# Kernel optimization log

Measured on AMD Instinct MI355X. Metric: run time of the kernel, lower is better.

The kernel has to match this reference:

```python
import jax, jax.numpy as jnp
import numpy as np

D_MODEL = 1024
H = 16
D_K = D_MODEL // H


def setup_inputs() -> dict:
    key = jax.random.key(0)
    ks = jax.random.split(key, 11)
    B, S = 4, 2048
    scale = 1.0 / np.sqrt(D_MODEL)
    inp = {
        "q": jax.random.normal(ks[0], (B, S, D_MODEL), jnp.float32),
        "k": jax.random.normal(ks[1], (B, S, D_MODEL), jnp.float32),
        "v": jax.random.normal(ks[2], (B, S, D_MODEL), jnp.float32),
        "wq": jax.random.normal(ks[3], (D_MODEL, D_MODEL), jnp.float32) * scale,
        "bq": jax.random.normal(ks[4], (D_MODEL,), jnp.float32) * 0.02,
        "wk": jax.random.normal(ks[5], (D_MODEL, D_MODEL), jnp.float32) * scale,
        "bk": jax.random.normal(ks[6], (D_MODEL,), jnp.float32) * 0.02,
        "wv": jax.random.normal(ks[7], (D_MODEL, D_MODEL), jnp.float32) * scale,
        "bv": jax.random.normal(ks[8], (D_MODEL,), jnp.float32) * 0.02,
        "wo": jax.random.normal(ks[9], (D_MODEL, D_MODEL), jnp.float32) * scale,
        "bo": jax.random.normal(ks[10], (D_MODEL,), jnp.float32) * 0.02,
    }
    return inp


def _split_heads(x):
    b, s, d = x.shape
    return x.reshape(b, s, H, D_K).transpose(0, 2, 1, 3)  # b h s k


def reference(q, k, v, wq, bq, wk, bk, wv, bv, wo, bo):
    # linear projections (torch Linear: x @ W^T + b; here weights stored as [in,out])
    qh = _split_heads(q @ wq + bq)
    kh = _split_heads(k @ wk + bk)
    vh = _split_heads(v @ wv + bv)
    scores = jnp.einsum('bhsk,bhtk->bhst', qh, kh) / np.sqrt(D_K)
    attn = jax.nn.softmax(scores, axis=-1)
    wv_ = jnp.einsum('bhst,bhtk->bhsk', attn, vh)
    b, h, s, dk = wv_.shape
    cv = wv_.transpose(0, 2, 1, 3).reshape(b, s, h * dk)
    return cv @ wo + bo
```

## Files before the change

### kernel.cpp

```cpp
#include <hip/hip_runtime.h>


#define DM 1024
#define SQL 2048

typedef __attribute__((ext_vector_type(4))) float floatx4;
typedef __attribute__((ext_vector_type(8))) __bf16 bf16x8;
typedef __attribute__((ext_vector_type(4))) __bf16 bf16x4;
typedef __attribute__((ext_vector_type(4))) unsigned int uintx4;

#define SW(row, chunk) (((row) << 6) + ((((chunk) ^ ((row) & 7))) << 3))

#define GLD(gaddr, laddr)                                                              \
  __builtin_amdgcn_global_load_lds(                                                    \
      (const __attribute__((address_space(1))) unsigned int*)(gaddr),                  \
      (__attribute__((address_space(3))) unsigned int*)(laddr), 16, 0, 0)

__device__ __forceinline__ unsigned short f2bf(float f) {
  unsigned int u = __float_as_uint(f);
  u += 0x7fffu + ((u >> 16) & 1u);
  return (unsigned short)(u >> 16);
}

__device__ __forceinline__ unsigned int pack_bf(float lo, float hi) {
  unsigned int a = __float_as_uint(lo) + 0x8000u;
  unsigned int b = __float_as_uint(hi) + 0x8000u;
  return __builtin_amdgcn_perm(b, a, 0x07060302u);
}

__device__ __forceinline__ bf16x8 pack8(floatx4 a, floatx4 b) {
  bf16x8 r;
  r[0] = (__bf16)a[0]; r[1] = (__bf16)a[1]; r[2] = (__bf16)a[2]; r[3] = (__bf16)a[3];
  r[4] = (__bf16)b[0]; r[5] = (__bf16)b[1]; r[6] = (__bf16)b[2]; r[7] = (__bf16)b[3];
  return r;
}

__global__ __launch_bounds__(256) void transpose4_kernel(
    const float* __restrict__ w0, const float* __restrict__ w1,
    const float* __restrict__ w2, const float* __restrict__ w3,
    unsigned short* __restrict__ t0, unsigned short* __restrict__ t1,
    unsigned short* __restrict__ t2, unsigned short* __restrict__ t3) {
  __shared__ unsigned short t[64][65];
  int z = blockIdx.z;
  const float* W = (z == 0) ? w0 : (z == 1) ? w1 : (z == 2) ? w2 : w3;
  unsigned short* Wt = (z == 0) ? t0 : (z == 1) ? t1 : (z == 2) ? t2 : t3;
  int tid = threadIdx.x;
  int n0 = blockIdx.x * 64, k0 = blockIdx.y * 64;
  for (int u = 0; u < 16; u++) {
    int idx = u * 256 + tid;
    int k = idx >> 6, n = idx & 63;
    t[k][n] = f2bf(W[(size_t)(k0 + k) * DM + n0 + n]);
  }
  __syncthreads();
  for (int u = 0; u < 16; u++) {
    int idx = u * 256 + tid;
    int n = idx >> 6, k = idx & 63;
    Wt[(size_t)(n0 + n) * DM + k0 + k] = t[k][n];
  }
}

__global__ __launch_bounds__(256) void convert3_kernel(
    const float* __restrict__ s0, const float* __restrict__ s1,
    const float* __restrict__ s2, unsigned short* __restrict__ d0,
    unsigned short* __restrict__ d1, unsigned short* __restrict__ d2) {
  int z = blockIdx.y;
  const float* S = (z == 0) ? s0 : (z == 1) ? s1 : s2;
  unsigned short* D = (z == 0) ? d0 : (z == 1) ? d1 : d2;
  int t = blockIdx.x * 256 + threadIdx.x;
  for (int u = 0; u < 8; u++) {
    int i = (u << 18) + t;
    float4 vv = ((const float4*)S)[i];
    uint2 p;
    p.x = pack_bf(vv.x, vv.y);
    p.y = pack_bf(vv.z, vv.w);
    ((uint2*)D)[i] = p;
  }
}

__device__ __forceinline__ void gemm_core_256x128(
    const unsigned short* __restrict__ A, const unsigned short* __restrict__ Bt,
    int m0, int n0, unsigned short* lds_a, unsigned short* lds_b,
    floatx4 acc[4][4]) {
  int tid = threadIdx.x;
  int wave = tid >> 6, lane = tid & 63;
  int quad = lane >> 4, c16 = lane & 15;
  int wm = wave >> 1, wn = wave & 1;
  int r8 = lane >> 3, l8 = lane & 7;
  int xch = (l8 ^ r8) << 3;

  int r7 = c16 & 7;
  int aoff0 = ((wm * 64 + c16) << 6) + ((quad ^ r7) << 3);
  int aoff1 = ((wm * 64 + c16) << 6) + (((4 + quad) ^ r7) << 3);
  int boff0 = ((wn * 64 + c16) << 6) + ((quad ^ r7) << 3);
  int boff1 = ((wn * 64 + c16) << 6) + (((4 + quad) ^ r7) << 3);

  int aq = wave * 4;
  int bq = wave * 2;

#define STG_A(bufp, kt, u) \
  GLD(&A[(size_t)(m0 + (aq + (u)) * 8 + r8) * DM + (kt) + xch], (bufp) + (aq + (u)) * 512)
#define STG_B(bufp, kt, u) \
  GLD(&Bt[(size_t)(n0 + (bq + (u)) * 8 + r8) * DM + (kt) + xch], (bufp) + (bq + (u)) * 512)

  const floatx4 fz = {0.f, 0.f, 0.f, 0.f};
#pragma unroll
  for (int i = 0; i < 4; i++)
#pragma unroll
    for (int j = 0; j < 4; j++) acc[i][j] = fz;

#pragma unroll
  for (int u = 0; u < 4; u++) STG_A(lds_a, 0, u);
  STG_B(lds_b, 0, 0);
  STG_B(lds_b, 0, 1);
#pragma unroll
  for (int u = 0; u < 4; u++) STG_A(lds_a + 16384, 64, u);
  STG_B(lds_b + 8192, 64, 0);
  STG_B(lds_b + 8192, 64, 1);

  int cur = 0;
#pragma unroll 1
  for (int t = 0; t < 16; ++t) {
    if (t < 15) asm volatile("s_waitcnt vmcnt(6)\n\ts_barrier" ::: "memory");
    else        asm volatile("s_waitcnt vmcnt(0)\n\ts_barrier" ::: "memory");

    const unsigned short* la = lds_a + cur * 16384;
    const unsigned short* lb = lds_b + cur * 8192;
    int stg = cur + 2;
    if (stg >= 3) stg -= 3;
    unsigned short* sa = lds_a + stg * 16384;
    unsigned short* sb = lds_b + stg * 8192;
    bool do_st = (t < 14);
    int kt2 = (t + 2) << 6;

    bf16x8 a_[2], b0[4], b1[4];

    a_[0] = *(const bf16x8*)&la[aoff0];
    a_[1] = *(const bf16x8*)&la[aoff0 + 1024];
    b0[0] = *(const bf16x8*)&lb[boff0];
    b0[1] = *(const bf16x8*)&lb[boff0 + 1024];
    b0[2] = *(const bf16x8*)&lb[boff0 + 2048];
    b0[3] = *(const bf16x8*)&lb[boff0 + 3072];
    if (do_st) { STG_A(sa, kt2, 0); STG_A(sa, kt2, 1); }
    __builtin_amdgcn_s_barrier();
    __builtin_amdgcn_s_setprio(1);
#pragma unroll
    for (int j = 0; j < 4; j++)
      acc[0][j] = __builtin_amdgcn_mfma_f32_16x16x32_bf16(a_[0], b0[j], acc[0][j], 0, 0, 0);
#pragma unroll
    for (int j = 0; j < 4; j++)
      acc[1][j] = __builtin_amdgcn_mfma_f32_16x16x32_bf16(a_[1], b0[j], acc[1][j], 0, 0, 0);
    __builtin_amdgcn_s_setprio(0);
    __builtin_amdgcn_s_barrier();

    a_[0] = *(const bf16x8*)&la[aoff0 + 2048];
    a_[1] = *(const bf16x8*)&la[aoff0 + 3072];
    if (do_st) { STG_A(sa, kt2, 2); STG_A(sa, kt2, 3); }
    __builtin_amdgcn_s_barrier();
    __builtin_amdgcn_s_setprio(1);
#pragma unroll
    for (int j = 0; j < 4; j++)
      acc[2][j] = __builtin_amdgcn_mfma_f32_16x16x32_bf16(a_[0], b0[j], acc[2][j], 0, 0, 0);
#pragma unroll
    for (int j = 0; j < 4; j++)
      acc[3][j] = __builtin_amdgcn_mfma_f32_16x16x32_bf16(a_[1], b0[j], acc[3][j], 0, 0, 0);
    __builtin_amdgcn_s_setprio(0);
    __builtin_amdgcn_s_barrier();

    a_[0] = *(const bf16x8*)&la[aoff1];
    a_[1] = *(const bf16x8*)&la[aoff1 + 1024];
    b1[0] = *(const bf16x8*)&lb[boff1];
    b1[1] = *(const bf16x8*)&lb[boff1 + 1024];
    b1[2] = *(const bf16x8*)&lb[boff1 + 2048];
    b1[3] = *(const bf16x8*)&lb[boff1 + 3072];
    if (do_st) { STG_B(sb, kt2, 0); STG_B(sb, kt2, 1); }
    __builtin_amdgcn_s_barrier();
    __builtin_amdgcn_s_setprio(1);
#pragma unroll
    for (int j = 0; j < 4; j++)
      acc[0][j] = __builtin_amdgcn_mfma_f32_16x16x32_bf16(a_[0], b1[j], acc[0][j], 0, 0, 0);
#pragma unroll
    for (int j = 0; j < 4; j++)
      acc[1][j] = __builtin_amdgcn_mfma_f32_16x16x32_bf16(a_[1], b1[j], acc[1][j], 0, 0, 0);
    __builtin_amdgcn_s_setprio(0);
    __builtin_amdgcn_s_barrier();

    a_[0] = *(const bf16x8*)&la[aoff1 + 2048];
    a_[1] = *(const bf16x8*)&la[aoff1 + 3072];
    __builtin_amdgcn_s_barrier();
    __builtin_amdgcn_s_setprio(1);
#pragma unroll
    for (int j = 0; j < 4; j++)
      acc[2][j] = __builtin_amdgcn_mfma_f32_16x16x32_bf16(a_[0], b1[j], acc[2][j], 0, 0, 0);
#pragma unroll
    for (int j = 0; j < 4; j++)
      acc[3][j] = __builtin_amdgcn_mfma_f32_16x16x32_bf16(a_[1], b1[j], acc[3][j], 0, 0, 0);
    __builtin_amdgcn_s_setprio(0);

    cur = cur + 1;
    if (cur >= 3) cur = 0;
  }
#undef STG_A
#undef STG_B
}

__global__ __launch_bounds__(512, 2) void gemm_qkv_kernel(
    const unsigned short* __restrict__ Aq, const unsigned short* __restrict__ Ak,
    const unsigned short* __restrict__ Av, const unsigned short* __restrict__ wqt,
    const unsigned short* __restrict__ wkt, const unsigned short* __restrict__ wvt,
    const float* __restrict__ bq, const float* __restrict__ bk,
    const float* __restrict__ bv, unsigned short* __restrict__ Qb,
    unsigned short* __restrict__ Kb, unsigned short* __restrict__ VtOut,
    float qscale) {
  __shared__ unsigned short lds_a[3 * 256 * 64];
  __shared__ unsigned short lds_b[3 * 128 * 64];

  int lin = blockIdx.x + (blockIdx.y << 3) + (blockIdx.z << 8);
  int swz = (lin & 7) * 96 + (lin >> 3);
  int z = swz >> 8, rem = swz & 255;
  int m0 = (rem >> 3) << 8;
  int n0 = (rem & 7) << 7;

  const unsigned short* A  = (z == 0) ? Aq : (z == 1) ? Ak : Av;
  const unsigned short* Bt = (z == 0) ? wqt : (z == 1) ? wkt : wvt;
  const float* bias = (z == 0) ? bq : (z == 1) ? bk : bv;

  floatx4 acc[4][4];
  gemm_core_256x128(A, Bt, m0, n0, lds_a, lds_b, acc);

  int tid = threadIdx.x;
  int wave = tid >> 6, lane = tid & 63;
  int quad = lane >> 4, c16 = lane & 15;
  int wm = wave >> 1, wn = wave & 1;

  float scale = (z == 0) ? qscale : 1.0f;
#pragma unroll
  for (int i = 0; i < 4; i++)
#pragma unroll
    for (int j = 0; j < 4; j++) {
      int gc = n0 + wn * 64 + j * 16 + c16;
      float bvv = bias[gc];
      float val[4];
#pragma unroll
      for (int r = 0; r < 4; r++) val[r] = (acc[i][j][r] + bvv) * scale;
      int gr0 = m0 + wm * 64 + i * 16 + quad * 4;
      if (z < 2) {
        unsigned short* O = (z == 0) ? Qb : Kb;
#pragma unroll
        for (int r = 0; r < 4; r++) O[(size_t)(gr0 + r) * DM + gc] = f2bf(val[r]);
      } else {
        int hh = gc >> 6, dd = gc & 63;
        int bidx = gr0 >> 11, srow = gr0 & 2047;
        int s6 = srow & 63;
        int c6 = (s6 & 32) | ((s6 & 8) << 1) | ((s6 & 4) << 1) | ((s6 & 16) >> 2) | (s6 & 3);
        int srowp = (srow & ~63) | c6;
        uint2 pk;
        pk.x = pack_bf(val[0], val[1]);
        pk.y = pack_bf(val[2], val[3]);
        *(uint2*)&VtOut[((size_t)(bidx * 16 + hh) * 64 + dd) * SQL + srowp] = pk;
      }
    }
}

__global__ __launch_bounds__(512, 2) void gemm_out_kernel(
    const unsigned short* __restrict__ A, const unsigned short* __restrict__ Bt,
    const float* __restrict__ bias, float* __restrict__ O) {
  __shared__ unsigned short lds_a[3 * 256 * 64];
  __shared__ unsigned short lds_b[3 * 128 * 64];

  int lin = blockIdx.x + (blockIdx.y << 3);
  int swz = (lin & 7) * 32 + (lin >> 3);
  int m0 = (swz >> 3) << 8;
  int n0 = (swz & 7) << 7;

  floatx4 acc[4][4];
  gemm_core_256x128(A, Bt, m0, n0, lds_a, lds_b, acc);

  int tid = threadIdx.x;
  int wave = tid >> 6, lane = tid & 63;
  int quad = lane >> 4, c16 = lane & 15;
  int wm = wave >> 1, wn = wave & 1;

#pragma unroll
  for (int i = 0; i < 4; i++)
#pragma unroll
    for (int j = 0; j < 4; j++) {
      int gc = n0 + wn * 64 + j * 16 + c16;
      float bvv = bias[gc];
      int gr0 = m0 + wm * 64 + i * 16 + quad * 4;
#pragma unroll
      for (int r = 0; r < 4; r++) O[(size_t)(gr0 + r) * DM + gc] = acc[i][j][r] + bvv;
    }
}

__global__ __launch_bounds__(256, 4) void attn_kernel(
    const unsigned short* __restrict__ Qb, const unsigned short* __restrict__ Kb,
    const unsigned short* __restrict__ Vt, unsigned short* __restrict__ Cv) {
  __shared__ unsigned short lds_k[2][64 * 64];
  __shared__ unsigned short lds_v[2][64 * 64];
  int tid = threadIdx.x;
  int wave = tid >> 6, lane = tid & 63;
  int quad = lane >> 4, c16 = lane & 15;
  int bh = blockIdx.x, qt = blockIdx.y;
  int b = bh >> 4, h = bh & 15;

  int sr0 = tid >> 3, sc = tid & 7;
  const unsigned short* kbase = &Kb[(size_t)(b * SQL) * DM + h * 64 + sc * 8];
  const unsigned short* vbase = &Vt[(size_t)(bh * 64) * SQL + sc * 8];

  bf16x8 qf[2][2];
  for (int i = 0; i < 2; i++)
    for (int ks = 0; ks < 2; ks++) {
      int gr = b * SQL + qt * 128 + wave * 32 + i * 16 + c16;
      qf[i][ks] = *(const bf16x8*)&Qb[(size_t)gr * DM + h * 64 + ks * 32 + quad * 8];
    }

  const floatx4 fzero = {0.f, 0.f, 0.f, 0.f};
  floatx4 acc[4][2];
  for (int dt = 0; dt < 4; dt++)
    for (int i = 0; i < 2; i++) acc[dt][i] = fzero;
  float l_[2] = {0.f, 0.f};

  for (int u = 0; u < 2; u++) {
    int r = sr0 + u * 32;
    *(uint4*)&lds_k[0][SW(r, sc)] = *(const uint4*)&kbase[(size_t)r * DM];
    *(uint4*)&lds_v[0][SW(r, sc)] = *(const uint4*)&vbase[(size_t)r * SQL];
  }
  __syncthreads();

  for (int t = 0; t < 32; t++) {
    int cur = t & 1;
    uint4 kreg[2], vreg[2];
    if (t + 1 < 32) {
      int t1 = (t + 1) * 64;
      for (int u = 0; u < 2; u++) {
        int r = sr0 + u * 32;
        kreg[u] = *(const uint4*)&kbase[(size_t)(t1 + r) * DM];
        vreg[u] = *(const uint4*)&vbase[(size_t)r * SQL + t1];
      }
    }

    floatx4 s[2][4];
    for (int i = 0; i < 2; i++)
      for (int jt = 0; jt < 4; jt++) s[i][jt] = fzero;
    for (int ks = 0; ks < 2; ks++) {
      bf16x8 kf[4];
      for (int jt = 0; jt < 4; jt++)
        kf[jt] = *(const bf16x8*)&lds_k[cur][SW(jt * 16 + c16, ks * 4 + quad)];
      for (int i = 0; i < 2; i++)
        for (int jt = 0; jt < 4; jt++)
          s[i][jt] = __builtin_amdgcn_mfma_f32_16x16x32_bf16(kf[jt], qf[i][ks], s[i][jt], 0, 0, 0);
    }

    bf16x8 pw[2][2];
    for (int i = 0; i < 2; i++) {
      float sum = l_[i];
      for (int jt = 0; jt < 4; jt++)
        for (int r = 0; r < 4; r++) {
          float p = __builtin_amdgcn_exp2f(s[i][jt][r]);
          s[i][jt][r] = p;
          sum += p;
        }
      l_[i] = sum;
      for (int ks = 0; ks < 2; ks++)
        pw[i][ks] = pack8(s[i][2 * ks], s[i][2 * ks + 1]);
    }

    for (int ks = 0; ks < 2; ks++) {
      for (int dt = 0; dt < 4; dt++) {
        bf16x8 av = *(const bf16x8*)&lds_v[cur][SW(dt * 16 + c16, ks * 4 + quad)];
        for (int i = 0; i < 2; i++)
          acc[dt][i] = __builtin_amdgcn_mfma_f32_16x16x32_bf16(
              av, pw[i][ks], acc[dt][i], 0, 0, 0);
      }
    }

    if (t + 1 < 32) {
      int nxt = cur ^ 1;
      for (int u = 0; u < 2; u++) {
        int r = sr0 + u * 32;
        *(uint4*)&lds_k[nxt][SW(r, sc)] = kreg[u];
        *(uint4*)&lds_v[nxt][SW(r, sc)] = vreg[u];
      }
    }
    __syncthreads();
  }

  for (int i = 0; i < 2; i++) {
    l_[i] += __shfl_xor(l_[i], 16);
    l_[i] += __shfl_xor(l_[i], 32);
    float inv = 1.f / l_[i];
    int gr = b * SQL + qt * 128 + wave * 32 + i * 16 + c16;
    for (int dt = 0; dt < 4; dt++) {
      bf16x4 o;
      o[0] = (__bf16)(acc[dt][i][0] * inv);
      o[1] = (__bf16)(acc[dt][i][1] * inv);
      o[2] = (__bf16)(acc[dt][i][2] * inv);
      o[3] = (__bf16)(acc[dt][i][3] * inv);
      *(bf16x4*)&Cv[(size_t)gr * DM + h * 64 + dt * 16 + quad * 4] = o;
    }
  }
}

extern "C" void kernel_launch(void* const* d_in, const int* in_sizes, int n_in,
                              void* d_out, int out_size, void* d_ws, size_t ws_size,
                              hipStream_t stream) {
  const float* q  = (const float*)d_in[0];
  const float* k  = (const float*)d_in[1];
  const float* v  = (const float*)d_in[2];
  const float* wq = (const float*)d_in[3];
  const float* bq = (const float*)d_in[4];
  const float* wk = (const float*)d_in[5];
  const float* bk = (const float*)d_in[6];
  const float* wv = (const float*)d_in[7];
  const float* bv = (const float*)d_in[8];
  const float* wo = (const float*)d_in[9];
  const float* bo = (const float*)d_in[10];
  float* out = (float*)d_out;

  char* ws = (char*)d_ws;
  unsigned short* wqt = (unsigned short*)(ws + (size_t)0);
  unsigned short* wkt = (unsigned short*)(ws + ((size_t)2 << 20));
  unsigned short* wvt = (unsigned short*)(ws + ((size_t)4 << 20));
  unsigned short* wot = (unsigned short*)(ws + ((size_t)6 << 20));
  unsigned short* Qb  = (unsigned short*)(ws + ((size_t)8 << 20));
  unsigned short* Kb  = (unsigned short*)(ws + ((size_t)24 << 20));
  unsigned short* Vt  = (unsigned short*)(ws + ((size_t)40 << 20));
  unsigned short* Cv  = (unsigned short*)(ws + ((size_t)56 << 20));
  unsigned short* Aq = (unsigned short*)d_out;
  unsigned short* Ak = (unsigned short*)d_out + ((size_t)8 << 20);
  unsigned short* Av = Cv;

  const float QSCALE = 0.125f * 1.44269504088896340736f;

  dim3 blk(256);
  transpose4_kernel<<<dim3(16, 16, 4), blk, 0, stream>>>(wq, wk, wv, wo, wqt, wkt, wvt, wot);
  convert3_kernel<<<dim3(1024, 3), blk, 0, stream>>>(q, k, v, Aq, Ak, Av);
  gemm_qkv_kernel<<<dim3(8, 32, 3), dim3(512), 0, stream>>>(Aq, Ak, Av, wqt, wkt, wvt,
                                                            bq, bk, bv, Qb, Kb, Vt, QSCALE);
  attn_kernel<<<dim3(64, 16), blk, 0, stream>>>(Qb, Kb, Vt, Cv);
  gemm_out_kernel<<<dim3(8, 32), dim3(512), 0, stream>>>(Cv, wot, bo, out);
}
```

Baseline: 346.5 us.

## Switch attention to 32x32x16 MFMA with direct global-to-LDS K/V loads

Rewrites the attention kernel's inner loop to use 32x32x16 bf16 MFMA tiles instead of 16x16x32. The V-transpose permutation in the projection epilogue changes to match the new operand layout. K/V tiles are now prefetched with global_load_lds straight into swizzled LDS rather than staged through registers. The change also adds s_setprio around the MFMA phases and lowers the occupancy hint to 3 blocks per CU. The aim is fewer MFMA issues, fewer LDS reads and less register staging, at the cost of larger accumulator register use.

After: 342.7 us. Within noise of the previous version (-1.1%).

```diff
diff --git a/kernel.cpp b/kernel.cpp
--- a/kernel.cpp
+++ b/kernel.cpp
@@ -5,9 +5,9 @@
 #define SQL 2048
 
 typedef __attribute__((ext_vector_type(4))) float floatx4;
+typedef __attribute__((ext_vector_type(16))) float floatx16;
 typedef __attribute__((ext_vector_type(8))) __bf16 bf16x8;
 typedef __attribute__((ext_vector_type(4))) __bf16 bf16x4;
-typedef __attribute__((ext_vector_type(4))) unsigned int uintx4;
 
 #define SW(row, chunk) (((row) << 6) + ((((chunk) ^ ((row) & 7))) << 3))
 
@@ -26,13 +26,6 @@
   unsigned int a = __float_as_uint(lo) + 0x8000u;
   unsigned int b = __float_as_uint(hi) + 0x8000u;
   return __builtin_amdgcn_perm(b, a, 0x07060302u);
-}
-
-__device__ __forceinline__ bf16x8 pack8(floatx4 a, floatx4 b) {
-  bf16x8 r;
-  r[0] = (__bf16)a[0]; r[1] = (__bf16)a[1]; r[2] = (__bf16)a[2]; r[3] = (__bf16)a[3];
-  r[4] = (__bf16)b[0]; r[5] = (__bf16)b[1]; r[6] = (__bf16)b[2]; r[7] = (__bf16)b[3];
-  return r;
 }
 
 __global__ __launch_bounds__(256) void transpose4_kernel(
@@ -251,7 +244,7 @@
         int hh = gc >> 6, dd = gc & 63;
         int bidx = gr0 >> 11, srow = gr0 & 2047;
         int s6 = srow & 63;
-        int c6 = (s6 & 32) | ((s6 & 8) << 1) | ((s6 & 4) << 1) | ((s6 & 16) >> 2) | (s6 & 3);
+        int c6 = (s6 & 51) | ((s6 & 4) << 1) | ((s6 & 8) >> 1);
         int srowp = (srow & ~63) | c6;
         uint2 pk;
         pk.x = pack_bf(val[0], val[1]);
@@ -292,113 +285,122 @@
     }
 }
 
-__global__ __launch_bounds__(256, 4) void attn_kernel(
+__global__ __launch_bounds__(256, 3) void attn_kernel(
     const unsigned short* __restrict__ Qb, const unsigned short* __restrict__ Kb,
     const unsigned short* __restrict__ Vt, unsigned short* __restrict__ Cv) {
   __shared__ unsigned short lds_k[2][64 * 64];
   __shared__ unsigned short lds_v[2][64 * 64];
   int tid = threadIdx.x;
   int wave = tid >> 6, lane = tid & 63;
-  int quad = lane >> 4, c16 = lane & 15;
+  int q31 = lane & 31, hl = lane >> 5;
   int bh = blockIdx.x, qt = blockIdx.y;
   int b = bh >> 4, h = bh & 15;
 
-  int sr0 = tid >> 3, sc = tid & 7;
-  const unsigned short* kbase = &Kb[(size_t)(b * SQL) * DM + h * 64 + sc * 8];
-  const unsigned short* vbase = &Vt[(size_t)(bh * 64) * SQL + sc * 8];
-
-  bf16x8 qf[2][2];
-  for (int i = 0; i < 2; i++)
-    for (int ks = 0; ks < 2; ks++) {
-      int gr = b * SQL + qt * 128 + wave * 32 + i * 16 + c16;
-      qf[i][ks] = *(const bf16x8*)&Qb[(size_t)gr * DM + h * 64 + ks * 32 + quad * 8];
-    }
-
-  const floatx4 fzero = {0.f, 0.f, 0.f, 0.f};
-  floatx4 acc[4][2];
-  for (int dt = 0; dt < 4; dt++)
-    for (int i = 0; i < 2; i++) acc[dt][i] = fzero;
-  float l_[2] = {0.f, 0.f};
-
+  int rl = lane >> 3;
+  int xsl = ((lane & 7) ^ rl) << 3;
+  const unsigned short* kg = &Kb[(size_t)(b * SQL + wave * 16 + rl) * DM + h * 64 + xsl];
+  const unsigned short* vg = &Vt[((size_t)(bh * 64) + wave * 16 + rl) * SQL + xsl];
+
+  bf16x8 qf[4];
+  int gr = b * SQL + qt * 128 + wave * 32 + q31;
+#pragma unroll
+  for (int s = 0; s < 4; s++)
+    qf[s] = *(const bf16x8*)&Qb[(size_t)gr * DM + h * 64 + s * 16 + hl * 8];
+
+  const floatx16 fz16 = {0.f, 0.f, 0.f, 0.f, 0.f, 0.f, 0.f, 0.f,
+                         0.f, 0.f, 0.f, 0.f, 0.f, 0.f, 0.f, 0.f};
+  floatx16 o[2];
+  o[0] = fz16; o[1] = fz16;
+  float l_ = 0.f;
+
+#pragma unroll
   for (int u = 0; u < 2; u++) {
-    int r = sr0 + u * 32;
-    *(uint4*)&lds_k[0][SW(r, sc)] = *(const uint4*)&kbase[(size_t)r * DM];
-    *(uint4*)&lds_v[0][SW(r, sc)] = *(const uint4*)&vbase[(size_t)r * SQL];
+    GLD(kg + (size_t)(u * 8) * DM, &lds_k[0][(wave * 16 + u * 8) << 6]);
+    GLD(vg + (size_t)(u * 8) * SQL, &lds_v[0][(wave * 16 + u * 8) << 6]);
   }
   __syncthreads();
 
+#pragma unroll 1
   for (int t = 0; t < 32; t++) {
-    int cur = t & 1;
-    uint4 kreg[2], vreg[2];
+    int cur = t & 1, nxt = cur ^ 1;
     if (t + 1 < 32) {
-      int t1 = (t + 1) * 64;
+      size_t koff = (size_t)((t + 1) * 64) * DM;
+      size_t voff = (size_t)((t + 1) * 64);
+#pragma unroll
       for (int u = 0; u < 2; u++) {
-        int r = sr0 + u * 32;
-        kreg[u] = *(const uint4*)&kbase[(size_t)(t1 + r) * DM];
-        vreg[u] = *(const uint4*)&vbase[(size_t)r * SQL + t1];
+        GLD(kg + koff + (size_t)(u * 8) * DM, &lds_k[nxt][(wave * 16 + u * 8) << 6]);
+        GLD(vg + voff + (size_t)(u * 8) * SQL, &lds_v[nxt][(wave * 16 + u * 8) << 6]);
       }
     }
 
-    floatx4 s[2][4];
-    for (int i = 0; i < 2; i++)
-      for (int jt = 0; jt < 4; jt++) s[i][jt] = fzero;
-    for (int ks = 0; ks < 2; ks++) {
-      bf16x8 kf[4];
-      for (int jt = 0; jt < 4; jt++)
-        kf[jt] = *(const bf16x8*)&lds_k[cur][SW(jt * 16 + c16, ks * 4 + quad)];
-      for (int i = 0; i < 2; i++)
-        for (int jt = 0; jt < 4; jt++)
-          s[i][jt] = __builtin_amdgcn_mfma_f32_16x16x32_bf16(kf[jt], qf[i][ks], s[i][jt], 0, 0, 0);
-    }
-
-    bf16x8 pw[2][2];
-    for (int i = 0; i < 2; i++) {
-      float sum = l_[i];
-      for (int jt = 0; jt < 4; jt++)
-        for (int r = 0; r < 4; r++) {
-          float p = __builtin_amdgcn_exp2f(s[i][jt][r]);
-          s[i][jt][r] = p;
-          sum += p;
+    floatx16 st[2];
+    __builtin_amdgcn_s_setprio(1);
+#pragma unroll
+    for (int j = 0; j < 2; j++) {
+      bf16x8 kf = *(const bf16x8*)&lds_k[cur][SW(j * 32 + q31, hl)];
+      st[j] = __builtin_amdgcn_mfma_f32_32x32x16_bf16(kf, qf[0], fz16, 0, 0, 0);
+    }
+#pragma unroll
+    for (int s = 1; s < 4; s++)
+#pragma unroll
+      for (int j = 0; j < 2; j++) {
+        bf16x8 kf = *(const bf16x8*)&lds_k[cur][SW(j * 32 + q31, 2 * s + hl)];
+        st[j] = __builtin_amdgcn_mfma_f32_32x32x16_bf16(kf, qf[s], st[j], 0, 0, 0);
+      }
+    __builtin_amdgcn_s_setprio(0);
+
+#pragma unroll
+    for (int j = 0; j < 2; j++)
+#pragma unroll
+      for (int r = 0; r < 16; r++) st[j][r] = __builtin_amdgcn_exp2f(st[j][r]);
+    float p0 = 0.f, p1 = 0.f, p2 = 0.f, p3 = 0.f;
+#pragma unroll
+    for (int r = 0; r < 16; r += 2) {
+      p0 += st[0][r]; p1 += st[0][r + 1];
+      p2 += st[1][r]; p3 += st[1][r + 1];
+    }
+    l_ += (p0 + p1) + (p2 + p3);
+
+    bf16x8 pb[2][2];
+#pragma unroll
+    for (int j = 0; j < 2; j++)
+#pragma unroll
+      for (int s2 = 0; s2 < 2; s2++) {
+        bf16x8 r;
+#pragma unroll
+        for (int e = 0; e < 8; e++) r[e] = (__bf16)st[j][s2 * 8 + e];
+        pb[j][s2] = r;
+      }
+
+    __builtin_amdgcn_s_setprio(1);
+#pragma unroll
+    for (int dt = 0; dt < 2; dt++)
+#pragma unroll
+      for (int j = 0; j < 2; j++)
+#pragma unroll
+        for (int s2 = 0; s2 < 2; s2++) {
+          bf16x8 av = *(const bf16x8*)&lds_v[cur][SW(dt * 32 + q31, j * 4 + s2 * 2 + hl)];
+          o[dt] = __builtin_amdgcn_mfma_f32_32x32x16_bf16(av, pb[j][s2], o[dt], 0, 0, 0);
         }
-      l_[i] = sum;
-      for (int ks = 0; ks < 2; ks++)
-        pw[i][ks] = pack8(s[i][2 * ks], s[i][2 * ks + 1]);
-    }
-
-    for (int ks = 0; ks < 2; ks++) {
-      for (int dt = 0; dt < 4; dt++) {
-        bf16x8 av = *(const bf16x8*)&lds_v[cur][SW(dt * 16 + c16, ks * 4 + quad)];
-        for (int i = 0; i < 2; i++)
-          acc[dt][i] = __builtin_amdgcn_mfma_f32_16x16x32_bf16(
-              av, pw[i][ks], acc[dt][i], 0, 0, 0);
-      }
-    }
-
-    if (t + 1 < 32) {
-      int nxt = cur ^ 1;
-      for (int u = 0; u < 2; u++) {
-        int r = sr0 + u * 32;
-        *(uint4*)&lds_k[nxt][SW(r, sc)] = kreg[u];
-        *(uint4*)&lds_v[nxt][SW(r, sc)] = vreg[u];
-      }
-    }
+    __builtin_amdgcn_s_setprio(0);
+
     __syncthreads();
   }
 
-  for (int i = 0; i < 2; i++) {
-    l_[i] += __shfl_xor(l_[i], 16);
-    l_[i] += __shfl_xor(l_[i], 32);
-    float inv = 1.f / l_[i];
-    int gr = b * SQL + qt * 128 + wave * 32 + i * 16 + c16;
-    for (int dt = 0; dt < 4; dt++) {
-      bf16x4 o;
-      o[0] = (__bf16)(acc[dt][i][0] * inv);
-      o[1] = (__bf16)(acc[dt][i][1] * inv);
-      o[2] = (__bf16)(acc[dt][i][2] * inv);
-      o[3] = (__bf16)(acc[dt][i][3] * inv);
-      *(bf16x4*)&Cv[(size_t)gr * DM + h * 64 + dt * 16 + quad * 4] = o;
-    }
-  }
+  l_ += __shfl_xor(l_, 32);
+  float inv = 1.f / l_;
+#pragma unroll
+  for (int dt = 0; dt < 2; dt++)
+#pragma unroll
+    for (int g = 0; g < 4; g++) {
+      bf16x4 ov;
+      ov[0] = (__bf16)(o[dt][4 * g + 0] * inv);
+      ov[1] = (__bf16)(o[dt][4 * g + 1] * inv);
+      ov[2] = (__bf16)(o[dt][4 * g + 2] * inv);
+      ov[3] = (__bf16)(o[dt][4 * g + 3] * inv);
+      int d0 = dt * 32 + g * 8 + hl * 4;
+      *(bf16x4*)&Cv[(size_t)gr * DM + h * 64 + d0] = ov;
+    }
 }
 
 extern "C" void kernel_launch(void* const* d_in, const int* in_sizes, int n_in,
```
